# Kernel tuning notes

Measured on AMD Instinct MI355X. Metric: run time of the kernel, lower is better.

## Reference

```python
import jax, jax.numpy as jnp
import numpy as np

N, IN_DIM, LDIM = 8192, 512, 256
NEG_SLOPE = 0.01  # torch F.leaky_relu default
EPS = 1e-10


def setup_inputs() -> dict:
    key = jax.random.key(0)
    k1, k2, k3, k4 = jax.random.split(key, 4)
    x = jax.random.normal(k1, (N, IN_DIM), dtype=jnp.float32)
    adj = jax.random.uniform(k2, (N, N), dtype=jnp.float32)
    # nn.Linear(in_dim, learning_dim, bias=False) weight: [learning_dim, in_dim]
    proj_w = jax.random.normal(k3, (LDIM, IN_DIM), dtype=jnp.float32) * (1.0 / np.sqrt(IN_DIM))
    # nn.init.uniform_(learn_w, a=0, b=1)
    learn_w = jax.random.uniform(k4, (LDIM,), dtype=jnp.float32)
    return {"x": x, "adj": adj, "proj_w": proj_w, "learn_w": learn_w}


def reference(x, adj, proj_w, learn_w):
    # x_hat = projection(x): [N, LDIM]
    x_hat = x @ proj_w.T
    # cosine-distance score: sum_d w_d * (1 - xn_i[d] * xn_j[d])
    #   = sum(w) - (xn * w) @ xn.T  -- avoids the N x N x D intermediate
    xn = x_hat / jnp.linalg.norm(x_hat, axis=-1, keepdims=True)  # [N, LDIM]
    scores = jnp.sum(learn_w) - jnp.einsum('id,jd->ij', xn * learn_w, xn)  # [N, N]
    out = jax.nn.leaky_relu(scores, NEG_SLOPE)
    out = out - jnp.max(out, axis=-1, keepdims=True)
    soft_adj = adj * jnp.exp(out)
    soft_adj = soft_adj / jnp.sum(soft_adj, axis=-1, keepdims=True) + EPS
    return soft_adj
```

## Files before the change

### kernel.cpp

```cpp
#include <hip/hip_runtime.h>
#include <stdint.h>

#define NN 8192
#define KDIM 512
#define LDIM 256

typedef short bf16x8 __attribute__((ext_vector_type(8)));
typedef short short8 __attribute__((ext_vector_type(8)));
typedef float f32x4 __attribute__((ext_vector_type(4)));
typedef unsigned short u16x4 __attribute__((ext_vector_type(4)));

__device__ __forceinline__ unsigned short f2bf(float f) {
  unsigned int u = __float_as_uint(f);
  u = (u + 0x7fffu + ((u >> 16) & 1u)) >> 16;
  return (unsigned short)u;
}
__device__ __forceinline__ float bf2f(unsigned short s) {
  return __uint_as_float(((unsigned int)s) << 16);
}

__device__ __forceinline__ void async_ld16(const unsigned short* g, void* l) {
  __builtin_amdgcn_global_load_lds(
      (const __attribute__((address_space(1))) unsigned int*)g,
      (__attribute__((address_space(3))) unsigned int*)l, 16, 0, 0);
}

__global__ __launch_bounds__(256) void cast_kernel(
    const float* __restrict__ x, const float* __restrict__ pw,
    unsigned short* __restrict__ xb, unsigned short* __restrict__ pwb) {
  const int i = blockIdx.x * 256 + threadIdx.x;
  float4 v = ((const float4*)x)[i];
  u16x4 o;
  o[0] = (short)f2bf(v.x); o[1] = (short)f2bf(v.y);
  o[2] = (short)f2bf(v.z); o[3] = (short)f2bf(v.w);
  ((u16x4*)xb)[i] = o;
  if (i < (LDIM * KDIM) / 4) {
    float4 w = ((const float4*)pw)[i];
    u16x4 ow;
    ow[0] = (short)f2bf(w.x); ow[1] = (short)f2bf(w.y);
    ow[2] = (short)f2bf(w.z); ow[3] = (short)f2bf(w.w);
    ((u16x4*)pwb)[i] = ow;
  }
}

__global__ __launch_bounds__(256) void norm_kernel(
    const float* __restrict__ xh, const float* __restrict__ w,
    unsigned short* __restrict__ Ab, unsigned short* __restrict__ Bb) {
  const int row = blockIdx.x;
  const int d = threadIdx.x;
  const float v = xh[row * LDIM + d];
  float ss = v * v;
#pragma unroll
  for (int m = 1; m < 64; m <<= 1) ss += __shfl_xor(ss, m);
  __shared__ float s4[4];
  if ((d & 63) == 0) s4[d >> 6] = ss;
  __syncthreads();
  const float tot = s4[0] + s4[1] + s4[2] + s4[3];
  const float inv = 1.0f / sqrtf(tot);
  const float xn = v * inv;
  Bb[row * LDIM + d] = f2bf(xn);
  Ab[row * LDIM + d] = f2bf(xn * w[d]);
}

template <int K, int MODE>
__global__ __launch_bounds__(256) void gemm_bt(
    const unsigned short* __restrict__ A,
    const unsigned short* __restrict__ B,
    float* __restrict__ C,
    unsigned short* __restrict__ T,
    const float* __restrict__ adj,
    float* __restrict__ rowsum,
    int ldC) {
  constexpr int SMEM_BYTES = (MODE == 0) ? 32768 : 128 * 132 * 4;
  __shared__ alignas(16) char sm[SMEM_BYTES];
  __shared__ float rs[128];

  const int tid = threadIdx.x;
  const int wave = tid >> 6;
  const int lane = tid & 63;
  const int quad = lane >> 4;
  const int l16 = lane & 15;
  const int wm = wave >> 1;
  const int wn = wave & 1;

  const size_t row0 = (size_t)blockIdx.y * 128;
  const size_t col0 = (size_t)blockIdx.x * 128;

  const int c0 = wave * 128 + lane;
  const int mA = c0 >> 2;
  const int kA = (c0 & 3) * 8;
  const unsigned short* Ag = A + (row0 + mA) * (size_t)K + kA;
  const unsigned short* Bg = B + (col0 + mA) * (size_t)K + kA;

  char* const a0d = sm + wave * 2048;
  char* const b0d = sm + 8192 + wave * 2048;
  char* const a1d = sm + 16384 + wave * 2048;
  char* const b1d = sm + 24576 + wave * 2048;

  f32x4 acc[4][4];
#pragma unroll
  for (int i = 0; i < 4; ++i)
#pragma unroll
    for (int j = 0; j < 4; ++j) acc[i][j] = (f32x4)(0.0f);

  auto stage = [&](char* Ad, char* Bd, int k0) {
    async_ld16(Ag + k0, Ad);
    async_ld16(Ag + 16 * (size_t)K + k0, Ad + 1024);
    async_ld16(Bg + k0, Bd);
    async_ld16(Bg + 16 * (size_t)K + k0, Bd + 1024);
  };
  auto compute = [&](const char* Ab_, const char* Bb_) {
    bf16x8 av[4], bv[4];
#pragma unroll
    for (int mt = 0; mt < 4; ++mt)
      av[mt] = *(const bf16x8*)(Ab_ + (wm * 64 + mt * 16 + l16) * 64 + quad * 16);
#pragma unroll
    for (int nt = 0; nt < 4; ++nt)
      bv[nt] = *(const bf16x8*)(Bb_ + (wn * 64 + nt * 16 + l16) * 64 + quad * 16);
#pragma unroll
    for (int mt = 0; mt < 4; ++mt)
#pragma unroll
      for (int nt = 0; nt < 4; ++nt)
        acc[mt][nt] = __builtin_amdgcn_mfma_f32_16x16x32_bf16(
            av[mt], bv[nt], acc[mt][nt], 0, 0, 0);
  };

  stage(a0d, b0d, 0);
  __syncthreads();
  for (int k0 = 0; k0 < K; k0 += 64) {
    if (k0 + 32 < K) stage(a1d, b1d, k0 + 32);
    compute(sm, sm + 8192);
    __syncthreads();
    if (k0 + 64 < K) stage(a0d, b0d, k0 + 64);
    if (k0 + 32 < K) compute(sm + 16384, sm + 24576);
    __syncthreads();
  }

  if constexpr (MODE == 0) {
#pragma unroll
    for (int mt = 0; mt < 4; ++mt)
#pragma unroll
      for (int nt = 0; nt < 4; ++nt)
#pragma unroll
        for (int r = 0; r < 4; ++r) {
          size_t gr = row0 + wm * 64 + mt * 16 + quad * 4 + r;
          size_t gc = col0 + wn * 64 + nt * 16 + l16;
          C[gr * (size_t)ldC + gc] = acc[mt][nt][r];
        }
  } else {
    float* trans = (float*)sm;
#pragma unroll
    for (int mt = 0; mt < 4; ++mt)
#pragma unroll
      for (int nt = 0; nt < 4; ++nt)
#pragma unroll
        for (int r = 0; r < 4; ++r)
          trans[(wm * 64 + mt * 16 + quad * 4 + r) * 132 +
                wn * 64 + nt * 16 + l16] = acc[mt][nt][r];
    __syncthreads();

    const int r16 = tid >> 1;
    const int h = tid & 1;
    const size_t gr = row0 + r16;
    const float4* arow = (const float4*)(adj + gr * NN + col0 + h * 64);
    const float4* drow = (const float4*)(trans + r16 * 132 + h * 64);
    f32x4 ps = (f32x4)(0.0f);
#pragma unroll
    for (int g = 0; g < 4; ++g) {
      float4 a4[4], d4[4];
#pragma unroll
      for (int q = 0; q < 4; ++q) {
        a4[q] = arow[g * 4 + q];
        d4[q] = drow[g * 4 + q];
      }
      float tv[16];
#pragma unroll
      for (int q = 0; q < 4; ++q) {
        tv[q * 4 + 0] = a4[q].x * __expf(-d4[q].x);
        tv[q * 4 + 1] = a4[q].y * __expf(-d4[q].y);
        tv[q * 4 + 2] = a4[q].z * __expf(-d4[q].z);
        tv[q * 4 + 3] = a4[q].w * __expf(-d4[q].w);
      }
      if constexpr (MODE == 1) {
        short8 p0, p1;
#pragma unroll
        for (int j = 0; j < 16; ++j) {
          unsigned short us = f2bf(tv[j]);
          ps[j & 3] += bf2f(us);
          if (j < 8) p0[j] = (short)us; else p1[j - 8] = (short)us;
        }
        short8* trow = (short8*)(T + gr * NN + col0 + h * 64 + g * 16);
        trow[0] = p0;
        trow[1] = p1;
      } else {
        float4 o[4];
#pragma unroll
        for (int j = 0; j < 16; ++j) {
          ps[j & 3] += tv[j];
          ((float*)o)[j] = tv[j];
        }
        float4* crow = (float4*)(C + gr * NN + col0 + h * 64 + g * 16);
#pragma unroll
        for (int q = 0; q < 4; ++q) crow[q] = o[q];
      }
    }
    float part = ps[0] + ps[1] + ps[2] + ps[3];
    part += __shfl_xor(part, 1);
    if (h == 0) rs[r16] = part;
    __syncthreads();
    if (tid < 128) atomicAdd(&rowsum[row0 + tid], rs[tid]);
  }
}

__global__ __launch_bounds__(256) void scale_bf16_kernel(
    const unsigned short* __restrict__ T, const float* __restrict__ rowsum,
    float* __restrict__ out) {
  const size_t i = (size_t)blockIdx.x * 256 + threadIdx.x;
  const int row = (int)(i >> 9);
  const float inv = 1.0f / rowsum[row];
  short8 t0 = ((const short8*)T)[i * 2];
  short8 t1 = ((const short8*)T)[i * 2 + 1];
  float4 o0, o1, o2, o3;
  o0.x = bf2f((unsigned short)t0[0]) * inv + 1e-10f;
  o0.y = bf2f((unsigned short)t0[1]) * inv + 1e-10f;
  o0.z = bf2f((unsigned short)t0[2]) * inv + 1e-10f;
  o0.w = bf2f((unsigned short)t0[3]) * inv + 1e-10f;
  o1.x = bf2f((unsigned short)t0[4]) * inv + 1e-10f;
  o1.y = bf2f((unsigned short)t0[5]) * inv + 1e-10f;
  o1.z = bf2f((unsigned short)t0[6]) * inv + 1e-10f;
  o1.w = bf2f((unsigned short)t0[7]) * inv + 1e-10f;
  o2.x = bf2f((unsigned short)t1[0]) * inv + 1e-10f;
  o2.y = bf2f((unsigned short)t1[1]) * inv + 1e-10f;
  o2.z = bf2f((unsigned short)t1[2]) * inv + 1e-10f;
  o2.w = bf2f((unsigned short)t1[3]) * inv + 1e-10f;
  o3.x = bf2f((unsigned short)t1[4]) * inv + 1e-10f;
  o3.y = bf2f((unsigned short)t1[5]) * inv + 1e-10f;
  o3.z = bf2f((unsigned short)t1[6]) * inv + 1e-10f;
  o3.w = bf2f((unsigned short)t1[7]) * inv + 1e-10f;
  float4* dst = (float4*)(out + i * 16);
  dst[0] = o0; dst[1] = o1; dst[2] = o2; dst[3] = o3;
}

__global__ __launch_bounds__(256) void scale_f32_kernel(
    float* __restrict__ t, const float* __restrict__ rowsum) {
  const size_t i = (size_t)blockIdx.x * 256 + threadIdx.x;
  const int row = (int)(i >> 11);
  float4 v = ((float4*)t)[i];
  const float inv = 1.0f / rowsum[row];
  v.x = v.x * inv + 1e-10f;
  v.y = v.y * inv + 1e-10f;
  v.z = v.z * inv + 1e-10f;
  v.w = v.w * inv + 1e-10f;
  ((float4*)t)[i] = v;
}

extern "C" void kernel_launch(void* const* d_in, const int* in_sizes, int n_in,
                              void* d_out, int out_size, void* d_ws, size_t ws_size,
                              hipStream_t stream) {
  (void)in_sizes; (void)n_in; (void)out_size;
  const float* x   = (const float*)d_in[0];
  const float* adj = (const float*)d_in[1];
  const float* pw  = (const float*)d_in[2];
  const float* lw  = (const float*)d_in[3];
  float* out = (float*)d_out;
  char* ws = (char*)d_ws;

  unsigned short* xb   = (unsigned short*)(ws);
  unsigned short* pwb  = (unsigned short*)(ws + 8388608);
  float*          xhat = (float*)(ws + 8650752);
  unsigned short* Ab   = (unsigned short*)(ws + 17039360);
  unsigned short* Bb   = (unsigned short*)(ws + 21233664);
  float*          rsum = (float*)(ws + 25427968);
  unsigned short* Tbuf = (unsigned short*)(ws + 25460736);
  const bool big_ws = ws_size >= 25460736ull + (size_t)NN * NN * 2ull;

  cast_kernel<<<(NN * KDIM) / (256 * 4), 256, 0, stream>>>(x, pw, xb, pwb);
  gemm_bt<KDIM, 0><<<dim3(2, 64), 256, 0, stream>>>(xb, pwb, xhat, nullptr, nullptr, nullptr, LDIM);
  norm_kernel<<<NN, 256, 0, stream>>>(xhat, lw, Ab, Bb);
  hipMemsetAsync(rsum, 0, NN * sizeof(float), stream);
  if (big_ws) {
    gemm_bt<LDIM, 1><<<dim3(64, 64), 256, 0, stream>>>(Ab, Bb, nullptr, Tbuf, adj, rsum, NN);
    scale_bf16_kernel<<<(NN * NN) / (16 * 256), 256, 0, stream>>>(Tbuf, rsum, out);
  } else {
    gemm_bt<LDIM, 2><<<dim3(64, 64), 256, 0, stream>>>(Ab, Bb, out, nullptr, adj, rsum, NN);
    scale_f32_kernel<<<(NN / 4) * (NN / 256), 256, 0, stream>>>(out, rsum);
  }
}
```

Measured before the change: 612.8 us.

## Load GEMM operands directly from global in fused score kernel, drop LDS staging

```diff
diff --git a/kernel.cpp b/kernel.cpp
--- a/kernel.cpp
+++ b/kernel.cpp
@@ -71,10 +71,6 @@
     const float* __restrict__ adj,
     float* __restrict__ rowsum,
     int ldC) {
-  constexpr int SMEM_BYTES = (MODE == 0) ? 32768 : 128 * 132 * 4;
-  __shared__ alignas(16) char sm[SMEM_BYTES];
-  __shared__ float rs[128];
-
   const int tid = threadIdx.x;
   const int wave = tid >> 6;
   const int lane = tid & 63;
@@ -86,57 +82,57 @@
   const size_t row0 = (size_t)blockIdx.y * 128;
   const size_t col0 = (size_t)blockIdx.x * 128;
 
-  const int c0 = wave * 128 + lane;
-  const int mA = c0 >> 2;
-  const int kA = (c0 & 3) * 8;
-  const unsigned short* Ag = A + (row0 + mA) * (size_t)K + kA;
-  const unsigned short* Bg = B + (col0 + mA) * (size_t)K + kA;
-
-  char* const a0d = sm + wave * 2048;
-  char* const b0d = sm + 8192 + wave * 2048;
-  char* const a1d = sm + 16384 + wave * 2048;
-  char* const b1d = sm + 24576 + wave * 2048;
-
   f32x4 acc[4][4];
 #pragma unroll
   for (int i = 0; i < 4; ++i)
 #pragma unroll
     for (int j = 0; j < 4; ++j) acc[i][j] = (f32x4)(0.0f);
 
-  auto stage = [&](char* Ad, char* Bd, int k0) {
-    async_ld16(Ag + k0, Ad);
-    async_ld16(Ag + 16 * (size_t)K + k0, Ad + 1024);
-    async_ld16(Bg + k0, Bd);
-    async_ld16(Bg + 16 * (size_t)K + k0, Bd + 1024);
-  };
-  auto compute = [&](const char* Ab_, const char* Bb_) {
-    bf16x8 av[4], bv[4];
-#pragma unroll
-    for (int mt = 0; mt < 4; ++mt)
-      av[mt] = *(const bf16x8*)(Ab_ + (wm * 64 + mt * 16 + l16) * 64 + quad * 16);
-#pragma unroll
-    for (int nt = 0; nt < 4; ++nt)
-      bv[nt] = *(const bf16x8*)(Bb_ + (wn * 64 + nt * 16 + l16) * 64 + quad * 16);
-#pragma unroll
-    for (int mt = 0; mt < 4; ++mt)
+  if constexpr (MODE == 0) {
+    __shared__ alignas(16) char sm[32768];
+    const int c0 = wave * 128 + lane;
+    const int mA = c0 >> 2;
+    const int kA = (c0 & 3) * 8;
+    const unsigned short* Ag = A + (row0 + mA) * (size_t)K + kA;
+    const unsigned short* Bg = B + (col0 + mA) * (size_t)K + kA;
+    char* const a0d = sm + wave * 2048;
+    char* const b0d = sm + 8192 + wave * 2048;
+    char* const a1d = sm + 16384 + wave * 2048;
+    char* const b1d = sm + 24576 + wave * 2048;
+
+    auto stage = [&](char* Ad, char* Bd, int k0) {
+      async_ld16(Ag + k0, Ad);
+      async_ld16(Ag + 16 * (size_t)K + k0, Ad + 1024);
+      async_ld16(Bg + k0, Bd);
+      async_ld16(Bg + 16 * (size_t)K + k0, Bd + 1024);
+    };
+    auto compute = [&](const char* Ab_, const char* Bb_) {
+      bf16x8 av[4], bv[4];
+#pragma unroll
+      for (int mt = 0; mt < 4; ++mt)
+        av[mt] = *(const bf16x8*)(Ab_ + (wm * 64 + mt * 16 + l16) * 64 + quad * 16);
 #pragma unroll
       for (int nt = 0; nt < 4; ++nt)
-        acc[mt][nt] = __builtin_amdgcn_mfma_f32_16x16x32_bf16(
-            av[mt], bv[nt], acc[mt][nt], 0, 0, 0);
-  };
-
-  stage(a0d, b0d, 0);
-  __syncthreads();
-  for (int k0 = 0; k0 < K; k0 += 64) {
-    if (k0 + 32 < K) stage(a1d, b1d, k0 + 32);
-    compute(sm, sm + 8192);
+        bv[nt] = *(const bf16x8*)(Bb_ + (wn * 64 + nt * 16 + l16) * 64 + quad * 16);
+#pragma unroll
+      for (int mt = 0; mt < 4; ++mt)
+#pragma unroll
+        for (int nt = 0; nt < 4; ++nt)
+          acc[mt][nt] = __builtin_amdgcn_mfma_f32_16x16x32_bf16(
+              av[mt], bv[nt], acc[mt][nt], 0, 0, 0);
+    };
+
+    stage(a0d, b0d, 0);
     __syncthreads();
-    if (k0 + 64 < K) stage(a0d, b0d, k0 + 64);
-    if (k0 + 32 < K) compute(sm + 16384, sm + 24576);
-    __syncthreads();
-  }
-
-  if constexpr (MODE == 0) {
+    for (int k0 = 0; k0 < K; k0 += 64) {
+      if (k0 + 32 < K) stage(a1d, b1d, k0 + 32);
+      compute(sm, sm + 8192);
+      __syncthreads();
+      if (k0 + 64 < K) stage(a0d, b0d, k0 + 64);
+      if (k0 + 32 < K) compute(sm + 16384, sm + 24576);
+      __syncthreads();
+    }
+
 #pragma unroll
     for (int mt = 0; mt < 4; ++mt)
 #pragma unroll
@@ -148,67 +144,66 @@
           C[gr * (size_t)ldC + gc] = acc[mt][nt][r];
         }
   } else {
-    float* trans = (float*)sm;
-#pragma unroll
-    for (int mt = 0; mt < 4; ++mt)
+    __shared__ float rs[2][128];
+    const unsigned short* Arow = A + (row0 + wm * 64 + l16) * (size_t)K + quad * 8;
+    const unsigned short* Brow = B + (col0 + wn * 64 + l16) * (size_t)K + quad * 8;
+
+#pragma unroll
+    for (int k0 = 0; k0 < K; k0 += 32) {
+      bf16x8 av[4], bv[4];
+#pragma unroll
+      for (int mt = 0; mt < 4; ++mt)
+        av[mt] = *(const bf16x8*)(Arow + (size_t)mt * 16 * K + k0);
 #pragma unroll
       for (int nt = 0; nt < 4; ++nt)
-#pragma unroll
-        for (int r = 0; r < 4; ++r)
-          trans[(wm * 64 + mt * 16 + quad * 4 + r) * 132 +
-                wn * 64 + nt * 16 + l16] = acc[mt][nt][r];
+        bv[nt] = *(const bf16x8*)(Brow + (size_t)nt * 16 * K + k0);
+#pragma unroll
+      for (int mt = 0; mt < 4; ++mt)
+#pragma unroll
+        for (int nt = 0; nt < 4; ++nt)
+          acc[mt][nt] = __builtin_amdgcn_mfma_f32_16x16x32_bf16(
+              bv[nt], av[mt], acc[mt][nt], 0, 0, 0);
+    }
+
+    float part[4] = {0.0f, 0.0f, 0.0f, 0.0f};
+#pragma unroll
+    for (int mt = 0; mt < 4; ++mt) {
+      const size_t gr = row0 + wm * 64 + mt * 16 + l16;
+      const float* arow = adj + gr * NN;
+#pragma unroll
+      for (int nt = 0; nt < 4; ++nt) {
+        const size_t gc = col0 + wn * 64 + nt * 16 + quad * 4;
+        float4 a4 = *(const float4*)(arow + gc);
+        f32x4 d = acc[mt][nt];
+        float t0 = a4.x * __expf(-d[0]);
+        float t1 = a4.y * __expf(-d[1]);
+        float t2 = a4.z * __expf(-d[2]);
+        float t3 = a4.w * __expf(-d[3]);
+        if constexpr (MODE == 1) {
+          u16x4 p;
+          p[0] = (short)f2bf(t0); p[1] = (short)f2bf(t1);
+          p[2] = (short)f2bf(t2); p[3] = (short)f2bf(t3);
+          part[mt] += bf2f(p[0]) + bf2f(p[1]) + bf2f(p[2]) + bf2f(p[3]);
+          *(u16x4*)(T + gr * NN + gc) = p;
+        } else {
+          part[mt] += t0 + t1 + t2 + t3;
+          float4 o; o.x = t0; o.y = t1; o.z = t2; o.w = t3;
+          *(float4*)(C + gr * NN + gc) = o;
+        }
+      }
+    }
+#pragma unroll
+    for (int mt = 0; mt < 4; ++mt) {
+      part[mt] += __shfl_xor(part[mt], 16);
+      part[mt] += __shfl_xor(part[mt], 32);
+    }
+    if (quad == 0) {
+#pragma unroll
+      for (int mt = 0; mt < 4; ++mt)
+        rs[wn][wm * 64 + mt * 16 + l16] = part[mt];
+    }
     __syncthreads();
-
-    const int r16 = tid >> 1;
-    const int h = tid & 1;
-    const size_t gr = row0 + r16;
-    const float4* arow = (const float4*)(adj + gr * NN + col0 + h * 64);
-    const float4* drow = (const float4*)(trans + r16 * 132 + h * 64);
-    f32x4 ps = (f32x4)(0.0f);
-#pragma unroll
-    for (int g = 0; g < 4; ++g) {
-      float4 a4[4], d4[4];
-#pragma unroll
-      for (int q = 0; q < 4; ++q) {
-        a4[q] = arow[g * 4 + q];
-        d4[q] = drow[g * 4 + q];
-      }
-      float tv[16];
-#pragma unroll
-      for (int q = 0; q < 4; ++q) {
-        tv[q * 4 + 0] = a4[q].x * __expf(-d4[q].x);
-        tv[q * 4 + 1] = a4[q].y * __expf(-d4[q].y);
-        tv[q * 4 + 2] = a4[q].z * __expf(-d4[q].z);
-        tv[q * 4 + 3] = a4[q].w * __expf(-d4[q].w);
-      }
-      if constexpr (MODE == 1) {
-        short8 p0, p1;
-#pragma unroll
-        for (int j = 0; j < 16; ++j) {
-          unsigned short us = f2bf(tv[j]);
-          ps[j & 3] += bf2f(us);
-          if (j < 8) p0[j] = (short)us; else p1[j - 8] = (short)us;
-        }
-        short8* trow = (short8*)(T + gr * NN + col0 + h * 64 + g * 16);
-        trow[0] = p0;
-        trow[1] = p1;
-      } else {
-        float4 o[4];
-#pragma unroll
-        for (int j = 0; j < 16; ++j) {
-          ps[j & 3] += tv[j];
-          ((float*)o)[j] = tv[j];
-        }
-        float4* crow = (float4*)(C + gr * NN + col0 + h * 64 + g * 16);
-#pragma unroll
-        for (int q = 0; q < 4; ++q) crow[q] = o[q];
-      }
-    }
-    float part = ps[0] + ps[1] + ps[2] + ps[3];
-    part += __shfl_xor(part, 1);
-    if (h == 0) rs[r16] = part;
-    __syncthreads();
-    if (tid < 128) atomicAdd(&rowsum[row0 + tid], rs[tid]);
+    if (tid < 128) atomicAdd(&rowsum[row0 + tid], rs[0][tid] + rs[1][tid]);
   }
 }
 
```

After: 676.8 us. +10.5%, slower.
